# Optimization experiments

Measured on AMD Instinct MI355X. Metric: run time of the kernel, lower is better.

The kernel has to match this reference:

```python
import jax, jax.numpy as jnp
import numpy as np

D_MODEL = 1472
N_HEADS = 6
D_KV = 64
INNER = N_HEADS * D_KV
NUM_BUCKETS = 32
MAX_DIST = 128


def _relative_position_bucket(relative_position, bidirectional=True,
                              num_buckets=NUM_BUCKETS, max_distance=MAX_DIST):
    ret = jnp.zeros_like(relative_position)
    if bidirectional:
        num_buckets //= 2
        ret = ret + (relative_position > 0).astype(jnp.int32) * num_buckets
        rel = jnp.abs(relative_position)
    else:
        rel = -jnp.minimum(relative_position, 0)
    max_exact = num_buckets // 2
    is_small = rel < max_exact
    rel_f = jnp.maximum(rel, 1).astype(jnp.float32)
    large = max_exact + (
        jnp.log(rel_f / max_exact) / np.log(max_distance / max_exact)
        * (num_buckets - max_exact)
    ).astype(jnp.int32)
    large = jnp.minimum(large, num_buckets - 1)
    return ret + jnp.where(is_small, rel, large)


def _position_bias(q_len, k_len, rel_bias):
    # rel_bias: [num_buckets, n_heads]
    ctx = jnp.arange(q_len)[:, None]
    mem = jnp.arange(k_len)[None, :]
    buckets = _relative_position_bucket(mem - ctx, bidirectional=True)
    values = rel_bias[buckets]                 # [Q, K, H]
    return jnp.transpose(values, (2, 0, 1))[None]  # [1, H, Q, K]


def setup_inputs() -> dict:
    key = jax.random.key(0)
    ks = jax.random.split(key, 8)
    B, S = 4, 2048
    scale = 0.02
    return {
        "kv_sequences": jax.random.normal(ks[0], (B, S, D_MODEL), jnp.float32),
        "q_sequences": jax.random.normal(ks[1], (B, S, D_MODEL), jnp.float32),
        "mask": jnp.zeros((B, 1, S, S), jnp.float32),
        "WQ": jax.random.normal(ks[2], (D_MODEL, INNER), jnp.float32) * scale,
        "WK": jax.random.normal(ks[3], (D_MODEL, INNER), jnp.float32) * scale,
        "WV": jax.random.normal(ks[4], (D_MODEL, INNER), jnp.float32) * scale,
        "WO": jax.random.normal(ks[5], (INNER, D_MODEL), jnp.float32) * scale,
        "rel_bias": jax.random.normal(ks[6], (NUM_BUCKETS, N_HEADS), jnp.float32) * scale,
    }


def reference(kv_sequences, q_sequences, mask, WQ, WK, WV, WO, rel_bias):
    B, Kl, _ = kv_sequences.shape
    Ql = q_sequences.shape[1]
    # projections -> [B, H, L, d_kv]
    q = (q_sequences @ WQ).reshape(B, Ql, N_HEADS, D_KV).transpose(0, 2, 1, 3)
    k = (kv_sequences @ WK).reshape(B, Kl, N_HEADS, D_KV).transpose(0, 2, 1, 3)
    v = (kv_sequences @ WV).reshape(B, Kl, N_HEADS, D_KV).transpose(0, 2, 1, 3)
    # T5-style: no 1/sqrt(d) scaling
    logits = jnp.einsum("bhqd,bhkd->bhqk", q, k)
    logits = logits + _position_bias(Ql, Kl, rel_bias)
    logits = logits + mask
    attn = jax.nn.softmax(logits.astype(jnp.float32), axis=-1).astype(logits.dtype)
    out = jnp.einsum("bhqk,bhkd->bhqd", attn, v)
    out = out.transpose(0, 2, 1, 3).reshape(B, Ql, INNER)
    return out @ WO
```

## Files before the change

### kernel.cpp

```cpp
#include <hip/hip_runtime.h>
#include <hip/hip_fp16.h>
#include <cstdint>

#define DM    1472
#define NH    6
#define DKV   64
#define INNER 384
#define BATCH 4
#define SEQ   2048
#define LOG2E 1.4426950408889634f

typedef __attribute__((ext_vector_type(8))) _Float16 half8;
typedef __attribute__((ext_vector_type(4))) _Float16 half4;
typedef __attribute__((ext_vector_type(4))) float f32x4;

__device__ __forceinline__ int swz64(int row, int b)  { return b ^ (((row >> 1) & 3) << 4); }
__device__ __forceinline__ int swz128(int row, int b) { return b ^ ((row & 7) << 4); }

__device__ __forceinline__ void gload16(const void* g, const void* l) {
  __builtin_amdgcn_global_load_lds((const __attribute__((address_space(1))) void*)g,
                                   (__attribute__((address_space(3))) void*)l, 16, 0, 0);
}

__global__ void prep_weights(const float* __restrict__ WQ, const float* __restrict__ WK,
                             const float* __restrict__ WV, const float* __restrict__ WO,
                             _Float16* __restrict__ WqT, _Float16* __restrict__ WkT,
                             _Float16* __restrict__ WvT, _Float16* __restrict__ WoT) {
  int idx = blockIdx.x * blockDim.x + threadIdx.x;
  const int per = DM * INNER;
  if (idx >= 4 * per) return;
  int which = idx / per;
  int i = idx - which * per;
  if (which < 3) {
    const float* W = which == 0 ? WQ : (which == 1 ? WK : WV);
    _Float16* T = which == 0 ? WqT : (which == 1 ? WkT : WvT);
    int k = i / INNER, n = i - (i / INNER) * INNER;
    T[(size_t)n * DM + k] = (_Float16)W[i];
  } else {
    int k = i / DM, n = i - (i / DM) * DM;
    WoT[(size_t)n * INNER + k] = (_Float16)WO[i];
  }
}

__global__ void prep_bias(const float* __restrict__ rel_bias, float* __restrict__ biasS) {
  int idx = blockIdx.x * blockDim.x + threadIdx.x;
  const int TOT = NH * 4 * 4104;
  if (idx >= TOT) return;
  int h = idx / (4 * 4104);
  int rem = idx - h * 4 * 4104;
  int cc = rem / 4104;
  int i = rem - cc * 4104;
  int j = i + cc; if (j > 4094) j = 4094;
  int d = j - 2047;
  int ret = d > 0 ? 16 : 0;
  int a = d < 0 ? -d : d;
  int bucket;
  if (a < 8) bucket = ret + a;
  else {
    int large;
    if      (a >= 91) large = 15;
    else if (a >= 64) large = 14;
    else if (a >= 46) large = 13;
    else if (a >= 32) large = 12;
    else if (a >= 23) large = 11;
    else if (a >= 16) large = 10;
    else if (a >= 12) large = 9;
    else              large = 8;
    bucket = ret + large;
  }
  biasS[idx] = rel_bias[bucket * NH + h] * LOG2E;
}

__global__ __launch_bounds__(256) void proj_gemm(
    const float* __restrict__ Xq, const float* __restrict__ Xkv,
    const _Float16* __restrict__ WqT, const _Float16* __restrict__ WkvT,
    _Float16* __restrict__ Qo, _Float16* __restrict__ Ko, _Float16* __restrict__ Vto) {
  const int bm = blockIdx.x, by = blockIdx.y;
  const bool isQ = by < 3;
  const float* __restrict__ X = isQ ? Xq : Xkv;
  const _Float16* __restrict__ WT = isQ ? (WqT + (size_t)by * 128 * DM)
                                        : (WkvT + (size_t)(by - 3) * 128 * DM);

  __shared__ alignas(16) float    As[2][128 * 32];
  __shared__ alignas(16) _Float16 Bs[2][128 * 32];

  const int tid = threadIdx.x;
  const int lane = tid & 63, wave = tid >> 6;
  const int wm = wave >> 1, wn = wave & 1;
  const int l15 = lane & 15, lg = lane >> 4;

  f32x4 acc[4][4] = {};

  const int aoff = 4 * ((lane & 7) ^ (lane >> 3));
  const float* asrc[4];
#pragma unroll
  for (int c = 0; c < 4; ++c)
    asrc[c] = X + (size_t)(bm * 128 + (wave * 4 + c) * 8 + (lane >> 3)) * DM + aoff;
  const int boff = 8 * ((lane & 3) ^ ((lane >> 3) & 3));
  const _Float16* bsrc[2];
#pragma unroll
  for (int c = 0; c < 2; ++c)
    bsrc[c] = WT + (size_t)((wave * 2 + c) * 16 + (lane >> 2)) * DM + boff;

  const int NT = DM / 32;

#pragma unroll
  for (int c = 0; c < 4; ++c)
    gload16(asrc[c], (const char*)&As[0][0] + (wave * 4 + c) * 1024);
#pragma unroll
  for (int c = 0; c < 2; ++c)
    gload16(bsrc[c], (const char*)&Bs[0][0] + (wave * 2 + c) * 1024);
  __syncthreads();

  for (int t = 0; t < NT; ++t) {
    if (t + 1 < NT) {
      const int nb = (t + 1) & 1;
      const int kf = (t + 1) * 32;
#pragma unroll
      for (int c = 0; c < 4; ++c)
        gload16(asrc[c] + kf, (const char*)&As[nb][0] + (wave * 4 + c) * 1024);
#pragma unroll
      for (int c = 0; c < 2; ++c)
        gload16(bsrc[c] + kf, (const char*)&Bs[nb][0] + (wave * 2 + c) * 1024);
    }

    const char* Ab = (const char*)&As[t & 1][0];
    const char* Bb = (const char*)&Bs[t & 1][0];
    half8 af[4], bf[4];
#pragma unroll
    for (int m = 0; m < 4; ++m) {
      int r = wm * 64 + m * 16 + l15;
      int s = (r & 7) << 4;
      f32x4 x0 = *(const f32x4*)(Ab + r * 128 + ((lg * 32) ^ s));
      f32x4 x1 = *(const f32x4*)(Ab + r * 128 + ((lg * 32 + 16) ^ s));
      half8 h;
#pragma unroll
      for (int j = 0; j < 4; ++j) { h[j] = (_Float16)x0[j]; h[4 + j] = (_Float16)x1[j]; }
      af[m] = h;
    }
#pragma unroll
    for (int n = 0; n < 4; ++n) {
      int r = wn * 64 + n * 16 + l15;
      bf[n] = *(const half8*)(Bb + r * 64 + ((lg * 16) ^ (((r >> 1) & 3) << 4)));
    }

    __builtin_amdgcn_s_setprio(1);
#pragma unroll
    for (int m = 0; m < 4; ++m)
#pragma unroll
      for (int n = 0; n < 4; ++n)
        acc[m][n] = __builtin_amdgcn_mfma_f32_16x16x32_f16(af[m], bf[n], acc[m][n], 0, 0, 0);
    __builtin_amdgcn_s_setprio(0);

    __syncthreads();
  }

#pragma unroll
  for (int m = 0; m < 4; ++m)
#pragma unroll
    for (int n = 0; n < 4; ++n)
#pragma unroll
      for (int r = 0; r < 4; ++r) {
        int gm = bm * 128 + wm * 64 + m * 16 + lg * 4 + r;
        int gnl = wn * 64 + n * 16 + l15;
        int b = gm >> 11, s = gm & 2047;
        float av = acc[m][n][r];
        if (isQ) {
          int gn = by * 128 + gnl;
          int h = gn >> 6, dd = gn & 63;
          Qo[((size_t)(b * NH + h) * SEQ + s) * DKV + dd] = (_Float16)(av * LOG2E);
        } else {
          int gn = (by - 3) * 128 + gnl;
          if (gn < INNER) {
            int h = gn >> 6, dd = gn & 63;
            Ko[((size_t)(b * NH + h) * SEQ + s) * DKV + dd] = (_Float16)av;
          } else {
            int gnv = gn - INNER;
            int h = gnv >> 6, dd = gnv & 63;
            Vto[((size_t)(b * NH + h) * DKV + dd) * SEQ + s] = (_Float16)av;
          }
        }
      }
}

__global__ __launch_bounds__(256, 3) void attn_kernel(
    const _Float16* __restrict__ Q, const _Float16* __restrict__ K, const _Float16* __restrict__ Vt,
    const float* __restrict__ biasS, const float* __restrict__ mask, _Float16* __restrict__ AO) {
  const int bid = blockIdx.x;
  const int g = (bid & 7) * 96 + (bid >> 3);
  const int bh = g >> 5, qb = g & 31;
  const int b = bh / NH, h = bh - b * NH;
  const int q0 = qb * 64;
  const int tid = threadIdx.x, lane = tid & 63, wave = tid >> 6;
  const int l15 = lane & 15, lg = lane >> 4;

  __shared__ alignas(16) _Float16 Ks[2][64 * 64];
  __shared__ alignas(16) _Float16 Vs[2][64 * 64];
  __shared__ alignas(16) _Float16 Ps[4][16 * 72];

  const size_t bhS = (size_t)bh * SEQ;
  const int qq = q0 + wave * 16 + l15;

  const _Float16* Qbase = Q + (bhS + q0 + wave * 16) * DKV;
  half8 qf0 = *(const half8*)(Qbase + (size_t)l15 * DKV + lg * 8);
  half8 qf1 = *(const half8*)(Qbase + (size_t)l15 * DKV + 32 + lg * 8);

  const float* maskrow = mask + (size_t)b * SEQ * SEQ + (size_t)qq * SEQ + lg * 4;
  const int c = (3 - l15) & 3;
  const float* bbase = biasS + (size_t)(h * 4 + c) * 4104 + (lg * 4 - qq + 2047 - c);

  float m_r = -1e30f, l_acc = 0.f;
  f32x4 oacc[4] = {};

  const int srow = tid >> 2;
  const int scb = (tid & 3) * 32;
  const _Float16* Ksrc = K + (bhS + srow) * DKV + (scb >> 1);
  const _Float16* Vsrc = Vt + ((size_t)bh * DKV + srow) * SEQ + (scb >> 1);

  {
    half8 k0v = *(const half8*)(Ksrc);
    half8 k1v = *(const half8*)(Ksrc + 8);
    half8 v0v = *(const half8*)(Vsrc);
    half8 v1v = *(const half8*)(Vsrc + 8);
    char* KsW = (char*)&Ks[0][0];
    char* VsW = (char*)&Vs[0][0];
    *(half8*)(KsW + srow * 128 + swz128(srow, scb)) = k0v;
    *(half8*)(KsW + srow * 128 + swz128(srow, scb + 16)) = k1v;
    *(half8*)(VsW + srow * 128 + swz128(srow, scb)) = v0v;
    *(half8*)(VsW + srow * 128 + swz128(srow, scb + 16)) = v1v;
  }

  f32x4 mc[4], bc[4];
#pragma unroll
  for (int nf = 0; nf < 4; ++nf) {
    mc[nf] = *(const f32x4*)(maskrow + nf * 16);
    bc[nf] = *(const f32x4*)(bbase + nf * 16);
  }

#pragma unroll 2
  for (int t = 0; t < SEQ / 64; ++t) {
    __syncthreads();
    const int kt = t * 64;
    const bool pre = (t + 1 < SEQ / 64);
    half8 knA, knB, vnA, vnB;
    f32x4 mn[4], bn[4];
    if (pre) {
      const _Float16* kp = Ksrc + (size_t)(kt + 64) * DKV;
      knA = *(const half8*)(kp);
      knB = *(const half8*)(kp + 8);
      const _Float16* vp = Vsrc + kt + 64;
      vnA = *(const half8*)(vp);
      vnB = *(const half8*)(vp + 8);
#pragma unroll
      for (int nf = 0; nf < 4; ++nf) {
        mn[nf] = *(const f32x4*)(maskrow + kt + 64 + nf * 16);
        bn[nf] = *(const f32x4*)(bbase + kt + 64 + nf * 16);
      }
    }
    const char* KsB = (const char*)&Ks[t & 1][0];
    const char* VsB = (const char*)&Vs[t & 1][0];
    char* PsB = (char*)&Ps[wave][0];

    f32x4 sacc[4] = {};
    __builtin_amdgcn_s_setprio(1);
#pragma unroll
    for (int nf = 0; nf < 4; ++nf) {
      int kr = nf * 16 + l15;
      half8 kf0 = *(const half8*)(KsB + kr * 128 + swz128(kr, lg * 16));
      half8 kf1 = *(const half8*)(KsB + kr * 128 + swz128(kr, 64 + lg * 16));
      sacc[nf] = __builtin_amdgcn_mfma_f32_16x16x32_f16(kf0, qf0, sacc[nf], 0, 0, 0);
      sacc[nf] = __builtin_amdgcn_mfma_f32_16x16x32_f16(kf1, qf1, sacc[nf], 0, 0, 0);
    }
    __builtin_amdgcn_s_setprio(0);

    float sv[4][4];
    float fm[4];
#pragma unroll
    for (int nf = 0; nf < 4; ++nf) {
#pragma unroll
      for (int r = 0; r < 4; ++r)
        sv[nf][r] = sacc[nf][r] + bc[nf][r] + mc[nf][r] * LOG2E;
      fm[nf] = fmaxf(fmaxf(sv[nf][0], sv[nf][1]), fmaxf(sv[nf][2], sv[nf][3]));
    }
    float mx = fmaxf(fmaxf(fm[0], fm[1]), fmaxf(fm[2], fm[3]));
    mx = fmaxf(mx, __shfl_xor(mx, 16));
    mx = fmaxf(mx, __shfl_xor(mx, 32));

    if (!__all(mx <= m_r + 8.0f)) {
      float mnew = fmaxf(m_r, mx);
      float sc_ = __builtin_amdgcn_exp2f(m_r - mnew);
      m_r = mnew;
      l_acc *= sc_;
      f32x4 scv;
#pragma unroll
      for (int r = 0; r < 4; ++r) scv[r] = __shfl(sc_, lg * 4 + r);
#pragma unroll
      for (int df = 0; df < 4; ++df) oacc[df] *= scv;
    }

    float rs = 0.f;
#pragma unroll
    for (int nf = 0; nf < 4; ++nf) {
      half4 ph;
#pragma unroll
      for (int r = 0; r < 4; ++r) {
        float p = __builtin_amdgcn_exp2f(sv[nf][r] - m_r);
        rs += p;
        ph[r] = (_Float16)p;
      }
      *(half4*)(PsB + l15 * 144 + nf * 32 + lg * 8) = ph;
    }
    l_acc += rs;

    __builtin_amdgcn_s_setprio(1);
#pragma unroll
    for (int ks = 0; ks < 2; ++ks) {
      half8 pa = *(const half8*)(PsB + l15 * 144 + ks * 64 + lg * 16);
#pragma unroll
      for (int df = 0; df < 4; ++df) {
        int vr = df * 16 + l15;
        half8 vb = *(const half8*)(VsB + vr * 128 + swz128(vr, ks * 64 + lg * 16));
        oacc[df] = __builtin_amdgcn_mfma_f32_16x16x32_f16(pa, vb, oacc[df], 0, 0, 0);
      }
    }
    __builtin_amdgcn_s_setprio(0);

    if (pre) {
      char* KsW = (char*)&Ks[(t + 1) & 1][0];
      char* VsW = (char*)&Vs[(t + 1) & 1][0];
      *(half8*)(KsW + srow * 128 + swz128(srow, scb)) = knA;
      *(half8*)(KsW + srow * 128 + swz128(srow, scb + 16)) = knB;
      *(half8*)(VsW + srow * 128 + swz128(srow, scb)) = vnA;
      *(half8*)(VsW + srow * 128 + swz128(srow, scb + 16)) = vnB;
#pragma unroll
      for (int nf = 0; nf < 4; ++nf) { mc[nf] = mn[nf]; bc[nf] = bn[nf]; }
    }
  }

  l_acc += __shfl_xor(l_acc, 16);
  l_acc += __shfl_xor(l_acc, 32);
  f32x4 lv;
#pragma unroll
  for (int r = 0; r < 4; ++r) lv[r] = __shfl(l_acc, lg * 4 + r);
#pragma unroll
  for (int df = 0; df < 4; ++df) {
    int dd = df * 16 + l15;
#pragma unroll
    for (int r = 0; r < 4; ++r) {
      int qrow = q0 + wave * 16 + lg * 4 + r;
      AO[((size_t)(b * SEQ + qrow)) * INNER + h * DKV + dd] = (_Float16)(oacc[df][r] / lv[r]);
    }
  }
}

__global__ __launch_bounds__(256) void out_gemm(
    const _Float16* __restrict__ A, const _Float16* __restrict__ BT, float* __restrict__ C) {
  __shared__ alignas(16) _Float16 As[2][128 * 32];
  __shared__ alignas(16) _Float16 Bs[2][64 * 32];

  const int tid = threadIdx.x, lane = tid & 63, wave = tid >> 6;
  const int wm = wave >> 1, wn = wave & 1;
  const int bm = blockIdx.x, bn = blockIdx.y;
  const int l15 = lane & 15, lg = lane >> 4;

  f32x4 acc[4][2] = {};
  const int arow = tid >> 1, aseg = tid & 1;
  const int brow = tid >> 2, bchunk = tid & 3;
  const _Float16* asrc = A + (size_t)(bm * 128 + arow) * INNER + aseg * 16;
  const _Float16* bsrc = BT + (size_t)(bn * 64 + brow) * INNER + bchunk * 8;

  const int NT = INNER / 32;

  {
    half8 a0 = *(const half8*)(asrc);
    half8 a1 = *(const half8*)(asrc + 8);
    half8 b0 = *(const half8*)(bsrc);
    char* AsW = (char*)&As[0][0];
    char* BsW = (char*)&Bs[0][0];
    *(half8*)(AsW + arow * 64 + swz64(arow, aseg * 32)) = a0;
    *(half8*)(AsW + arow * 64 + swz64(arow, aseg * 32 + 16)) = a1;
    *(half8*)(BsW + brow * 64 + swz64(brow, bchunk * 16)) = b0;
  }

  for (int t = 0; t < NT; ++t) {
    __syncthreads();
    const bool pre = (t + 1 < NT);
    half8 na0, na1, nb0;
    if (pre) {
      const int kn = (t + 1) * 32;
      na0 = *(const half8*)(asrc + kn);
      na1 = *(const half8*)(asrc + kn + 8);
      nb0 = *(const half8*)(bsrc + kn);
    }

    const char* AsB = (const char*)&As[t & 1][0];
    const char* BsB = (const char*)&Bs[t & 1][0];
    half8 af[4], bf[2];
#pragma unroll
    for (int m = 0; m < 4; ++m) {
      int r = wm * 64 + m * 16 + l15;
      af[m] = *(const half8*)(AsB + r * 64 + swz64(r, lg * 16));
    }
#pragma unroll
    for (int n = 0; n < 2; ++n) {
      int r = wn * 32 + n * 16 + l15;
      bf[n] = *(const half8*)(BsB + r * 64 + swz64(r, lg * 16));
    }
    __builtin_amdgcn_s_setprio(1);
#pragma unroll
    for (int m = 0; m < 4; ++m)
#pragma unroll
      for (int n = 0; n < 2; ++n)
        acc[m][n] = __builtin_amdgcn_mfma_f32_16x16x32_f16(af[m], bf[n], acc[m][n], 0, 0, 0);
    __builtin_amdgcn_s_setprio(0);

    if (pre) {
      char* AsW = (char*)&As[(t + 1) & 1][0];
      char* BsW = (char*)&Bs[(t + 1) & 1][0];
      *(half8*)(AsW + arow * 64 + swz64(arow, aseg * 32)) = na0;
      *(half8*)(AsW + arow * 64 + swz64(arow, aseg * 32 + 16)) = na1;
      *(half8*)(BsW + brow * 64 + swz64(brow, bchunk * 16)) = nb0;
    }
  }

#pragma unroll
  for (int m = 0; m < 4; ++m)
#pragma unroll
    for (int n = 0; n < 2; ++n)
#pragma unroll
      for (int r = 0; r < 4; ++r) {
        int gm = bm * 128 + wm * 64 + m * 16 + lg * 4 + r;
        int gn = bn * 64 + wn * 32 + n * 16 + l15;
        C[(size_t)gm * DM + gn] = acc[m][n][r];
      }
}

extern "C" void kernel_launch(void* const* d_in, const int* in_sizes, int n_in,
                              void* d_out, int out_size, void* d_ws, size_t ws_size,
                              hipStream_t stream) {
  const float* kv   = (const float*)d_in[0];
  const float* qs   = (const float*)d_in[1];
  const float* mask = (const float*)d_in[2];
  const float* WQ   = (const float*)d_in[3];
  const float* WK   = (const float*)d_in[4];
  const float* WV   = (const float*)d_in[5];
  const float* WO   = (const float*)d_in[6];
  const float* rb   = (const float*)d_in[7];
  float* out = (float*)d_out;
  char* ws = (char*)d_ws;

  const size_t WT_BYTES  = (size_t)INNER * DM * 2;
  const size_t QKV_BYTES = (size_t)BATCH * NH * SEQ * DKV * 2;
  _Float16* WqT = (_Float16*)(ws);
  _Float16* WkT = (_Float16*)(ws + WT_BYTES);
  _Float16* WvT = (_Float16*)(ws + 2 * WT_BYTES);
  _Float16* WoT = (_Float16*)(ws + 3 * WT_BYTES);
  _Float16* Qh  = (_Float16*)(ws + 4 * WT_BYTES);
  _Float16* Kh  = (_Float16*)(ws + 4 * WT_BYTES + QKV_BYTES);
  _Float16* Vth = (_Float16*)(ws + 4 * WT_BYTES + 2 * QKV_BYTES);
  _Float16* AO  = (_Float16*)(ws + 4 * WT_BYTES + 3 * QKV_BYTES);
  float* biasS  = (float*)(ws + 4 * WT_BYTES + 4 * QKV_BYTES);

  hipLaunchKernelGGL(prep_weights, dim3((4 * DM * INNER + 255) / 256), dim3(256), 0, stream,
                     WQ, WK, WV, WO, WqT, WkT, WvT, WoT);
  hipLaunchKernelGGL(prep_bias, dim3((NH * 4 * 4104 + 255) / 256), dim3(256), 0, stream, rb, biasS);
  hipLaunchKernelGGL(proj_gemm, dim3(64, 9), dim3(256), 0, stream,
                     qs, kv, WqT, WkT, Qh, Kh, Vth);
  hipLaunchKernelGGL(attn_kernel, dim3(768), dim3(256), 0, stream,
                     Qh, Kh, Vth, biasS, mask, AO);
  hipLaunchKernelGGL(out_gemm, dim3(64, 23), dim3(256), 0, stream, AO, WoT, out);
}
```

Measured before the change: 194.6 us.

## Use direct global-to-LDS loads and software-pipeline QK^T one tile ahead

```diff
diff --git a/kernel.cpp b/kernel.cpp
--- a/kernel.cpp
+++ b/kernel.cpp
@@ -15,7 +15,6 @@
 typedef __attribute__((ext_vector_type(4))) float f32x4;
 
 __device__ __forceinline__ int swz64(int row, int b)  { return b ^ (((row >> 1) & 3) << 4); }
-__device__ __forceinline__ int swz128(int row, int b) { return b ^ ((row & 7) << 4); }
 
 __device__ __forceinline__ void gload16(const void* g, const void* l) {
   __builtin_amdgcn_global_load_lds((const __attribute__((address_space(1))) void*)g,
@@ -193,8 +192,9 @@
   const int q0 = qb * 64;
   const int tid = threadIdx.x, lane = tid & 63, wave = tid >> 6;
   const int l15 = lane & 15, lg = lane >> 4;
-
-  __shared__ alignas(16) _Float16 Ks[2][64 * 64];
+  const int NT = SEQ / 64;
+
+  __shared__ alignas(16) _Float16 Ks[3][64 * 64];
   __shared__ alignas(16) _Float16 Vs[2][64 * 64];
   __shared__ alignas(16) _Float16 Ps[4][16 * 72];
 
@@ -212,75 +212,84 @@
   float m_r = -1e30f, l_acc = 0.f;
   f32x4 oacc[4] = {};
 
-  const int srow = tid >> 2;
-  const int scb = (tid & 3) * 32;
-  const _Float16* Ksrc = K + (bhS + srow) * DKV + (scb >> 1);
-  const _Float16* Vsrc = Vt + ((size_t)bh * DKV + srow) * SEQ + (scb >> 1);
-
-  {
-    half8 k0v = *(const half8*)(Ksrc);
-    half8 k1v = *(const half8*)(Ksrc + 8);
-    half8 v0v = *(const half8*)(Vsrc);
-    half8 v1v = *(const half8*)(Vsrc + 8);
-    char* KsW = (char*)&Ks[0][0];
-    char* VsW = (char*)&Vs[0][0];
-    *(half8*)(KsW + srow * 128 + swz128(srow, scb)) = k0v;
-    *(half8*)(KsW + srow * 128 + swz128(srow, scb + 16)) = k1v;
-    *(half8*)(VsW + srow * 128 + swz128(srow, scb)) = v0v;
-    *(half8*)(VsW + srow * 128 + swz128(srow, scb + 16)) = v1v;
-  }
-
-  f32x4 mc[4], bc[4];
+  const int rl = lane >> 3;
+  const int sw = ((lane & 7) ^ rl) * 8;
+  const _Float16* Kd0 = K + (bhS + wave * 16 + rl) * DKV + sw;
+  const _Float16* Kd1 = Kd0 + 8 * DKV;
+  const _Float16* Vd0 = Vt + ((size_t)bh * DKV + wave * 16 + rl) * SEQ + sw;
+  const _Float16* Vd1 = Vd0 + 8 * SEQ;
+  char* KsB = (char*)&Ks[0][0];
+  char* VsB = (char*)&Vs[0][0];
+  char* PsB = (char*)&Ps[wave][0];
+  const int dmaLds = wave * 2048;
+
+  gload16(Kd0, KsB + dmaLds);
+  gload16(Kd1, KsB + dmaLds + 1024);
+  gload16(Kd0 + 64 * DKV, KsB + 8192 + dmaLds);
+  gload16(Kd1 + 64 * DKV, KsB + 8192 + dmaLds + 1024);
+  gload16(Vd0, VsB + dmaLds);
+  gload16(Vd1, VsB + dmaLds + 1024);
+
+  f32x4 mA[4], mB[4];
+#pragma unroll
+  for (int nf = 0; nf < 4; ++nf) mA[nf] = *(const f32x4*)(maskrow + nf * 16);
+
+  __syncthreads();
+
+  f32x4 sA[4] = {}, sB[4] = {};
+  __builtin_amdgcn_s_setprio(1);
 #pragma unroll
   for (int nf = 0; nf < 4; ++nf) {
-    mc[nf] = *(const f32x4*)(maskrow + nf * 16);
-    bc[nf] = *(const f32x4*)(bbase + nf * 16);
-  }
-
-#pragma unroll 2
-  for (int t = 0; t < SEQ / 64; ++t) {
-    __syncthreads();
-    const int kt = t * 64;
-    const bool pre = (t + 1 < SEQ / 64);
-    half8 knA, knB, vnA, vnB;
-    f32x4 mn[4], bn[4];
-    if (pre) {
-      const _Float16* kp = Ksrc + (size_t)(kt + 64) * DKV;
-      knA = *(const half8*)(kp);
-      knB = *(const half8*)(kp + 8);
-      const _Float16* vp = Vsrc + kt + 64;
-      vnA = *(const half8*)(vp);
-      vnB = *(const half8*)(vp + 8);
+    int kr = nf * 16 + l15;
+    const char* rb = KsB + kr * 128;
+    half8 kf0 = *(const half8*)(rb + ((lg ^ (kr & 7)) << 4));
+    half8 kf1 = *(const half8*)(rb + (((4 + lg) ^ (kr & 7)) << 4));
+    sA[nf] = __builtin_amdgcn_mfma_f32_16x16x32_f16(kf0, qf0, sA[nf], 0, 0, 0);
+    sA[nf] = __builtin_amdgcn_mfma_f32_16x16x32_f16(kf1, qf1, sA[nf], 0, 0, 0);
+  }
+  __builtin_amdgcn_s_setprio(0);
+
+  auto body = [&](int t, f32x4 (&sC)[4], f32x4 (&sN)[4], f32x4 (&mC)[4], f32x4 (&mN)[4]) {
+    const int nt1 = t + 1, nt2 = t + 2;
+    if (nt2 < NT) {
+      char* kb = KsB + (nt2 % 3) * 8192 + dmaLds;
+      gload16(Kd0 + (size_t)nt2 * 64 * DKV, kb);
+      gload16(Kd1 + (size_t)nt2 * 64 * DKV, kb + 1024);
+    }
+    if (nt1 < NT) {
+      char* vb_ = VsB + (nt1 & 1) * 8192 + dmaLds;
+      gload16(Vd0 + nt1 * 64, vb_);
+      gload16(Vd1 + nt1 * 64, vb_ + 1024);
+#pragma unroll
+      for (int nf = 0; nf < 4; ++nf)
+        mN[nf] = *(const f32x4*)(maskrow + nt1 * 64 + nf * 16);
+    }
+
+#pragma unroll
+    for (int nf = 0; nf < 4; ++nf) sN[nf] = (f32x4){0.f, 0.f, 0.f, 0.f};
+    if (nt1 < NT) {
+      const char* Kb = KsB + (nt1 % 3) * 8192;
+      __builtin_amdgcn_s_setprio(1);
 #pragma unroll
       for (int nf = 0; nf < 4; ++nf) {
-        mn[nf] = *(const f32x4*)(maskrow + kt + 64 + nf * 16);
-        bn[nf] = *(const f32x4*)(bbase + kt + 64 + nf * 16);
+        int kr = nf * 16 + l15;
+        const char* rb = Kb + kr * 128;
+        half8 kf0 = *(const half8*)(rb + ((lg ^ (kr & 7)) << 4));
+        half8 kf1 = *(const half8*)(rb + (((4 + lg) ^ (kr & 7)) << 4));
+        sN[nf] = __builtin_amdgcn_mfma_f32_16x16x32_f16(kf0, qf0, sN[nf], 0, 0, 0);
+        sN[nf] = __builtin_amdgcn_mfma_f32_16x16x32_f16(kf1, qf1, sN[nf], 0, 0, 0);
       }
-    }
-    const char* KsB = (const char*)&Ks[t & 1][0];
-    const char* VsB = (const char*)&Vs[t & 1][0];
-    char* PsB = (char*)&Ps[wave][0];
-
-    f32x4 sacc[4] = {};
-    __builtin_amdgcn_s_setprio(1);
+      __builtin_amdgcn_s_setprio(0);
+    }
+
+    float fm[4];
 #pragma unroll
     for (int nf = 0; nf < 4; ++nf) {
-      int kr = nf * 16 + l15;
-      half8 kf0 = *(const half8*)(KsB + kr * 128 + swz128(kr, lg * 16));
-      half8 kf1 = *(const half8*)(KsB + kr * 128 + swz128(kr, 64 + lg * 16));
-      sacc[nf] = __builtin_amdgcn_mfma_f32_16x16x32_f16(kf0, qf0, sacc[nf], 0, 0, 0);
-      sacc[nf] = __builtin_amdgcn_mfma_f32_16x16x32_f16(kf1, qf1, sacc[nf], 0, 0, 0);
-    }
-    __builtin_amdgcn_s_setprio(0);
-
-    float sv[4][4];
-    float fm[4];
-#pragma unroll
-    for (int nf = 0; nf < 4; ++nf) {
+      f32x4 bv = *(const f32x4*)(bbase + t * 64 + nf * 16);
 #pragma unroll
       for (int r = 0; r < 4; ++r)
-        sv[nf][r] = sacc[nf][r] + bc[nf][r] + mc[nf][r] * LOG2E;
-      fm[nf] = fmaxf(fmaxf(sv[nf][0], sv[nf][1]), fmaxf(sv[nf][2], sv[nf][3]));
+        sC[nf][r] = sC[nf][r] + bv[r] + mC[nf][r] * LOG2E;
+      fm[nf] = fmaxf(fmaxf(sC[nf][0], sC[nf][1]), fmaxf(sC[nf][2], sC[nf][3]));
     }
     float mx = fmaxf(fmaxf(fm[0], fm[1]), fmaxf(fm[2], fm[3]));
     mx = fmaxf(mx, __shfl_xor(mx, 16));
@@ -304,7 +313,7 @@
       half4 ph;
 #pragma unroll
       for (int r = 0; r < 4; ++r) {
-        float p = __builtin_amdgcn_exp2f(sv[nf][r] - m_r);
+        float p = __builtin_amdgcn_exp2f(sC[nf][r] - m_r);
         rs += p;
         ph[r] = (_Float16)p;
       }
@@ -312,6 +321,7 @@
     }
     l_acc += rs;
 
+    const char* Vb = VsB + (t & 1) * 8192;
     __builtin_amdgcn_s_setprio(1);
 #pragma unroll
     for (int ks = 0; ks < 2; ++ks) {
@@ -319,22 +329,18 @@
 #pragma unroll
       for (int df = 0; df < 4; ++df) {
         int vr = df * 16 + l15;
-        half8 vb = *(const half8*)(VsB + vr * 128 + swz128(vr, ks * 64 + lg * 16));
-        oacc[df] = __builtin_amdgcn_mfma_f32_16x16x32_f16(pa, vb, oacc[df], 0, 0, 0);
+        half8 vv = *(const half8*)(Vb + vr * 128 + (((ks * 4 + lg) ^ (vr & 7)) << 4));
+        oacc[df] = __builtin_amdgcn_mfma_f32_16x16x32_f16(pa, vv, oacc[df], 0, 0, 0);
       }
     }
     __builtin_amdgcn_s_setprio(0);
 
-    if (pre) {
-      char* KsW = (char*)&Ks[(t + 1) & 1][0];
-      char* VsW = (char*)&Vs[(t + 1) & 1][0];
-      *(half8*)(KsW + srow * 128 + swz128(srow, scb)) = knA;
-      *(half8*)(KsW + srow * 128 + swz128(srow, scb + 16)) = knB;
-      *(half8*)(VsW + srow * 128 + swz128(srow, scb)) = vnA;
-      *(half8*)(VsW + srow * 128 + swz128(srow, scb + 16)) = vnB;
-#pragma unroll
-      for (int nf = 0; nf < 4; ++nf) { mc[nf] = mn[nf]; bc[nf] = bn[nf]; }
-    }
+    __syncthreads();
+  };
+
+  for (int tt = 0; tt < NT / 2; ++tt) {
+    body(2 * tt,     sA, sB, mA, mB);
+    body(2 * tt + 1, sB, sA, mB, mA);
   }
 
   l_acc += __shfl_xor(l_acc, 16);
@@ -364,47 +370,45 @@
   const int l15 = lane & 15, lg = lane >> 4;
 
   f32x4 acc[4][2] = {};
-  const int arow = tid >> 1, aseg = tid & 1;
-  const int brow = tid >> 2, bchunk = tid & 3;
-  const _Float16* asrc = A + (size_t)(bm * 128 + arow) * INNER + aseg * 16;
-  const _Float16* bsrc = BT + (size_t)(bn * 64 + brow) * INNER + bchunk * 8;
+
+  const int rl4 = (lane >> 2) & 3;
+  const int soff = ((lane & 3) ^ rl4) * 8;
+  const _Float16* ad0 = A + (size_t)(bm * 128 + (wave * 2) * 16 + (lane >> 2)) * INNER + soff;
+  const _Float16* ad1 = ad0 + (size_t)16 * INNER;
+  const _Float16* bd0 = BT + (size_t)(bn * 64 + wave * 16 + (lane >> 2)) * INNER + soff;
+  char* AsB = (char*)&As[0][0];
+  char* BsB = (char*)&Bs[0][0];
+  const int aLds = wave * 2048;
+  const int bLds = wave * 1024;
 
   const int NT = INNER / 32;
 
-  {
-    half8 a0 = *(const half8*)(asrc);
-    half8 a1 = *(const half8*)(asrc + 8);
-    half8 b0 = *(const half8*)(bsrc);
-    char* AsW = (char*)&As[0][0];
-    char* BsW = (char*)&Bs[0][0];
-    *(half8*)(AsW + arow * 64 + swz64(arow, aseg * 32)) = a0;
-    *(half8*)(AsW + arow * 64 + swz64(arow, aseg * 32 + 16)) = a1;
-    *(half8*)(BsW + brow * 64 + swz64(brow, bchunk * 16)) = b0;
-  }
+  gload16(ad0, AsB + aLds);
+  gload16(ad1, AsB + aLds + 1024);
+  gload16(bd0, BsB + bLds);
+  __syncthreads();
 
   for (int t = 0; t < NT; ++t) {
-    __syncthreads();
-    const bool pre = (t + 1 < NT);
-    half8 na0, na1, nb0;
-    if (pre) {
-      const int kn = (t + 1) * 32;
-      na0 = *(const half8*)(asrc + kn);
-      na1 = *(const half8*)(asrc + kn + 8);
-      nb0 = *(const half8*)(bsrc + kn);
-    }
-
-    const char* AsB = (const char*)&As[t & 1][0];
-    const char* BsB = (const char*)&Bs[t & 1][0];
+    if (t + 1 < NT) {
+      const int nb = (t + 1) & 1;
+      const int kf = (t + 1) * 32;
+      gload16(ad0 + kf, AsB + nb * 8192 + aLds);
+      gload16(ad1 + kf, AsB + nb * 8192 + aLds + 1024);
+      gload16(bd0 + kf, BsB + nb * 4096 + bLds);
+    }
+
+    const char* Ab = AsB + (t & 1) * 8192;
+    const char* Bb = BsB + (t & 1) * 4096;
     half8 af[4], bf[2];
 #pragma unroll
     for (int m = 0; m < 4; ++m) {
       int r = wm * 64 + m * 16 + l15;
-      af[m] = *(const half8*)(AsB + r * 64 + swz64(r, lg * 16));
+      af[m] = *(const half8*)(Ab + r * 64 + (((lg ^ (r & 3))) << 4));
     }
 #pragma unroll
     for (int n = 0; n < 2; ++n) {
       int r = wn * 32 + n * 16 + l15;
-      bf[n] = *(const half8*)(BsB + r * 64 + swz64(r, lg * 16));
+      bf[n] = *(const half8*)(Bb + r * 64 + (((lg ^ (r & 3))) << 4));
     }
     __builtin_amdgcn_s_setprio(1);
 #pragma unroll
@@ -414,13 +418,7 @@
         acc[m][n] = __builtin_amdgcn_mfma_f32_16x16x32_f16(af[m], bf[n], acc[m][n], 0, 0, 0);
     __builtin_amdgcn_s_setprio(0);
 
-    if (pre) {
-      char* AsW = (char*)&As[(t + 1) & 1][0];
-      char* BsW = (char*)&Bs[(t + 1) & 1][0];
-      *(half8*)(AsW + arow * 64 + swz64(arow, aseg * 32)) = na0;
-      *(half8*)(AsW + arow * 64 + swz64(arow, aseg * 32 + 16)) = na1;
-      *(half8*)(BsW + brow * 64 + swz64(brow, bchunk * 16)) = nb0;
-    }
+    __syncthreads();
   }
 
 #pragma unroll
```

New measurement: 193.7 us. No clear change (-0.5%).
